# Optimization experiments

Measured on AMD Instinct MI355X. Metric: run time of the kernel, lower is better.

The kernel has to match this reference:

```python
import jax, jax.numpy as jnp
import numpy as np

N_NODES = 100000
N_EDGES = 1600000
F_IN = 128
HID = 64
EPS = 1e-5


def setup_inputs() -> dict:
    key = jax.random.key(0)
    ks = jax.random.split(key, 16)
    x = jax.random.normal(ks[0], (N_NODES, F_IN), dtype=jnp.float32)
    edge_index = jax.random.randint(ks[1], (2, N_EDGES), 0, N_NODES, dtype=jnp.int64)
    inp = {"x": x, "edge_index": edge_index}
    # GCN layers: layer 0 maps F_IN->HID, layers 1,2 map HID->HID
    dims = [(F_IN, HID), (HID, HID), (HID, HID)]
    for i, (fi, fo) in enumerate(dims):
        inp[f"W{i}"] = jax.random.normal(ks[2 + i], (fi, fo), dtype=jnp.float32) / np.sqrt(fi)
        inp[f"b{i}"] = jnp.zeros((fo,), dtype=jnp.float32)
        inp[f"g{i}"] = jnp.ones((fo,), dtype=jnp.float32)
        inp[f"bt{i}"] = jnp.zeros((fo,), dtype=jnp.float32)
    inp["lw1"] = jax.random.normal(ks[8], (HID, HID // 2), dtype=jnp.float32) / np.sqrt(HID)
    inp["lb1"] = jnp.zeros((HID // 2,), dtype=jnp.float32)
    inp["lw2"] = jax.random.normal(ks[9], (HID // 2, 1), dtype=jnp.float32) / np.sqrt(HID // 2)
    inp["lb2"] = jnp.zeros((1,), dtype=jnp.float32)
    return inp


def _gcn_norm(edge_index, n_nodes):
    # add self loops, symmetric normalization D^{-1/2}(A+I)D^{-1/2}
    loops = jnp.arange(n_nodes, dtype=edge_index.dtype)
    src = jnp.concatenate([edge_index[0], loops])
    dst = jnp.concatenate([edge_index[1], loops])
    deg = jax.ops.segment_sum(jnp.ones_like(dst, dtype=jnp.float32), dst, num_segments=n_nodes)
    dinv = jax.lax.rsqrt(deg)  # deg >= 1 thanks to self loops
    norm = dinv[src] * dinv[dst]  # [E+N]
    return src, dst, norm


def reference(x, edge_index, W0, b0, g0, bt0, W1, b1, g1, bt1, W2, b2, g2, bt2, lw1, lb1, lw2, lb2):
    n = x.shape[0]
    src, dst, norm = _gcn_norm(edge_index, n)
    layers = [(W0, b0, g0, bt0), (W1, b1, g1, bt1), (W2, b2, g2, bt2)]
    h = x
    for W, b, g, bt in layers:
        hw = h @ W                                  # [N, H] dense GEMM
        msg = hw[src] * norm[:, None]               # gather + scale, [E+N, H]
        agg = jax.ops.segment_sum(msg, dst, num_segments=n) + b  # scatter-add
        # BatchNorm1d (training-mode batch stats, biased var)
        mu = agg.mean(axis=0)
        var = agg.var(axis=0)
        h = (agg - mu) * jax.lax.rsqrt(var + EPS) * g + bt
        h = jax.nn.relu(h)                          # dropout = identity (inference)
    h = jax.nn.relu(h @ lw1 + lb1)
    out = h @ lw2 + lb2                             # [N, 1]
    return out[:, 0]
```

## Files before the change

### kernel.cpp

```cpp
#include <hip/hip_runtime.h>
#include <hip/hip_fp16.h>

#define HIDW 64
#define EPSV 1e-5f
#define CAP 32
#define GRP 512
#define CHUNK 4096
#define PSLOTS 40
#define NBIN_MAX 256
#define NCHUNK_MAX 512
#define NSLOT 64
#define OVFR 32768

__global__ __launch_bounds__(256) void k_zero(int* __restrict__ deg, int* __restrict__ ovfcnt,
                                              float* __restrict__ stats, int n) {
    int i = blockIdx.x * 256 + threadIdx.x;
    if (i < n) deg[i] = 0;
    if (i < 2) ovfcnt[i] = 0;
    if (i < 3 * NSLOT * 128) stats[i] = 0.f;
}

__global__ __launch_bounds__(256) void k_part(const int* __restrict__ srcv, const int* __restrict__ dstv,
                                              int2* __restrict__ pairs, unsigned char* __restrict__ cnts,
                                              int2* __restrict__ ovfl, int* __restrict__ ovfcnt,
                                              int e, int nchunk, int nbin) {
    __shared__ int lcnt[NBIN_MAX];
    int tid = threadIdx.x;
    int chunk = blockIdx.x;
    for (int i = tid; i < nbin; i += 256) lcnt[i] = 0;
    __syncthreads();
    int base = chunk * CHUNK;
#pragma unroll
    for (int t = 0; t < CHUNK / 256; ++t) {
        int i = base + t * 256 + tid;
        if (i < e) {
            int s = srcv[i];
            int d = dstv[i];
            int k = d >> 9;
            int slot = atomicAdd(&lcnt[k], 1);
            if (slot < PSLOTS) {
                pairs[((size_t)k * nchunk + chunk) * PSLOTS + slot] = make_int2(s, d);
            } else {
                int o = atomicAdd(&ovfcnt[0], 1);
                if (o < OVFR) ovfl[o] = make_int2(s, d);
            }
        }
    }
    __syncthreads();
    for (int i = tid; i < nbin; i += 256)
        cnts[(size_t)i * nchunk + chunk] = (unsigned char)min(lcnt[i], PSLOTS);
}

__global__ __launch_bounds__(256) void k_own(const int2* __restrict__ pairs, const unsigned char* __restrict__ cnts,
                                             int* __restrict__ deg, unsigned char* __restrict__ bcnt,
                                             int* __restrict__ csr, int2* __restrict__ ovfl,
                                             int* __restrict__ ovfcnt, int n, int nchunk) {
    __shared__ int lcnt[GRP];
    __shared__ int bkt[GRP * CAP];
    __shared__ unsigned char scnt[NCHUNK_MAX];
    int g = blockIdx.x;
    int tid = threadIdx.x;
    int nbase = g << 9;
    int nloc = min(GRP, n - nbase);
    for (int i = tid; i < GRP; i += 256) lcnt[i] = 0;
    for (int i = tid; i < nchunk; i += 256) scnt[i] = cnts[(size_t)g * nchunk + i];
    __syncthreads();
    const int2* pb = pairs + (size_t)g * nchunk * PSLOTS;
    int tot = nchunk * PSLOTS;
    for (int i = tid; i < tot; i += 256) {
        int c = i / PSLOTS;
        int s = i - c * PSLOTS;
        if (s < (int)scnt[c]) {
            int2 p = pb[i];
            int loc = p.y - nbase;
            int pos = atomicAdd(&lcnt[loc], 1);
            if (pos < CAP) {
                bkt[loc * CAP + pos] = p.x;
            } else {
                int o = atomicAdd(&ovfcnt[1], 1);
                if (o < OVFR) ovfl[OVFR + o] = p;
            }
        }
    }
    __syncthreads();
    int* csrb = csr + (size_t)nbase * CAP;
    for (int i = tid; i < nloc * CAP; i += 256) csrb[i] = bkt[i];
    for (int i = tid; i < nloc; i += 256) {
        int c = lcnt[i];
        deg[nbase + i] = c;
        bcnt[nbase + i] = (unsigned char)min(c, CAP);
    }
}

__global__ __launch_bounds__(256) void k_ovfdeg(const int2* __restrict__ ovfl, const int* __restrict__ ovfcnt,
                                                int* __restrict__ deg) {
    int m0 = min(ovfcnt[0], OVFR);
    for (int i = threadIdx.x; i < m0; i += 256) atomicAdd(&deg[ovfl[i].y], 1);
}

__global__ __launch_bounds__(256) void k_ovf(const __half* __restrict__ hw, const int2* __restrict__ ovfl,
                                             const int* __restrict__ ovfcnt, const int* __restrict__ deg,
                                             float* __restrict__ agg) {
    int m0 = min(ovfcnt[0], OVFR);
    int m1 = min(ovfcnt[1], OVFR);
    int tot = m0 + m1;
    if (tot == 0) return;
    int lane = threadIdx.x & 63;
    int w = (blockIdx.x * 256 + threadIdx.x) >> 6;
    for (; w < tot; w += gridDim.x * 4) {
        int2 p = (w < m0) ? ovfl[w] : ovfl[OVFR + (w - m0)];
        float wt = rsqrtf(1.0f + (float)deg[p.y]);
        atomicAdd(&agg[(size_t)p.y * HIDW + lane], __half2float(hw[(size_t)p.x * HIDW + lane]) * wt);
    }
}

__global__ __launch_bounds__(256) void k_count(const int* __restrict__ dstv, int* __restrict__ deg, int e) {
    int i = blockIdx.x * 256 + threadIdx.x;
    if (i < e) atomicAdd(&deg[dstv[i]], 1);
}

__global__ __launch_bounds__(256) void k_scan1(const int* __restrict__ deg, int* __restrict__ off,
                                               int* __restrict__ bsum, int n) {
    __shared__ int s[256];
    int tid = threadIdx.x;
    int i = blockIdx.x * 256 + tid;
    int v = (i < n) ? deg[i] : 0;
    s[tid] = v;
    __syncthreads();
    for (int o = 1; o < 256; o <<= 1) {
        int t = (tid >= o) ? s[tid - o] : 0;
        __syncthreads();
        s[tid] += t;
        __syncthreads();
    }
    if (i < n) off[i] = s[tid] - v;
    if (tid == 255) bsum[blockIdx.x] = s[255];
}

__global__ __launch_bounds__(512) void k_scan2(int* __restrict__ bsum, int nb) {
    __shared__ int s[512];
    int tid = threadIdx.x;
    int v = (tid < nb) ? bsum[tid] : 0;
    s[tid] = v;
    __syncthreads();
    for (int o = 1; o < 512; o <<= 1) {
        int t = (tid >= o) ? s[tid - o] : 0;
        __syncthreads();
        s[tid] += t;
        __syncthreads();
    }
    if (tid < nb) bsum[tid] = s[tid] - v;
}

__global__ __launch_bounds__(256) void k_scan3(int* __restrict__ off, const int* __restrict__ bsum, int n) {
    int i = blockIdx.x * 256 + threadIdx.x;
    if (i < n) off[i] += bsum[blockIdx.x];
}

__global__ __launch_bounds__(256) void k_fill2(const int* __restrict__ srcv, const int* __restrict__ dstv,
                                               int* __restrict__ roff, int* __restrict__ csr, int e) {
    int i = blockIdx.x * 256 + threadIdx.x;
    if (i < e) {
        int d = dstv[i];
        int p = atomicAdd(&roff[d], 1);
        csr[p] = srcv[i];
    }
}

template <int K, bool BN>
__global__ __launch_bounds__(256) void k_gemm(const float* __restrict__ h, const float* __restrict__ W,
                                              __half* __restrict__ hw, int n,
                                              const float* __restrict__ st, const float* __restrict__ g,
                                              const float* __restrict__ bt, float invn,
                                              const int* __restrict__ deg) {
    constexpr int KP = K + 4;
    constexpr int KQ = K / 4;
    __shared__ float sH[64 * KP];
    __shared__ float sW[K * 64];
    __shared__ float sM[128];
    __shared__ float sSc[HIDW];
    __shared__ float sSh[HIDW];
    int tid = threadIdx.x;
    int node0 = blockIdx.x * 64;

    if (BN) {
        if (tid < 128) {
            float t = 0.f;
#pragma unroll 8
            for (int s = 0; s < NSLOT; ++s) t += st[s * 128 + tid];
            sM[tid] = t;
        }
        __syncthreads();
        if (tid < HIDW) {
            float mu = sM[tid] * invn;
            float var = sM[HIDW + tid] * invn - mu * mu;
            var = fmaxf(var, 0.f);
            float rstd = rsqrtf(var + EPSV);
            float sc = rstd * g[tid];
            sSc[tid] = sc;
            sSh[tid] = bt[tid] - mu * sc;
        }
        __syncthreads();
    }

    for (int i = tid; i < K * 16; i += 256)
        ((float4*)sW)[i] = ((const float4*)W)[i];
    for (int i = tid; i < 64 * KQ; i += 256) {
        int row = i / KQ, kq = i % KQ;
        int nn = node0 + row;
        if (nn >= n) nn = n - 1;
        float4 v = ((const float4*)h)[(size_t)nn * KQ + kq];
        if (BN) {
            int c = 4 * kq;
            v.x = fmaxf(fmaf(v.x, sSc[c + 0], sSh[c + 0]), 0.f);
            v.y = fmaxf(fmaf(v.y, sSc[c + 1], sSh[c + 1]), 0.f);
            v.z = fmaxf(fmaf(v.z, sSc[c + 2], sSh[c + 2]), 0.f);
            v.w = fmaxf(fmaf(v.w, sSc[c + 3], sSh[c + 3]), 0.f);
        }
        ((float4*)(sH + row * KP))[kq] = v;
    }
    __syncthreads();

    int tx = tid & 15;
    int ny = tid >> 4;
    const float* hbase = sH + (4 * ny) * KP;

    float acc[4][4];
#pragma unroll
    for (int j = 0; j < 4; ++j)
#pragma unroll
        for (int c = 0; c < 4; ++c) acc[j][c] = 0.f;

#pragma unroll 2
    for (int kq = 0; kq < KQ; ++kq) {
        float4 w0 = ((const float4*)(sW + (4 * kq + 0) * 64))[tx];
        float4 w1 = ((const float4*)(sW + (4 * kq + 1) * 64))[tx];
        float4 w2 = ((const float4*)(sW + (4 * kq + 2) * 64))[tx];
        float4 w3 = ((const float4*)(sW + (4 * kq + 3) * 64))[tx];
#pragma unroll
        for (int j = 0; j < 4; ++j) {
            float4 hv = ((const float4*)(hbase + j * KP))[kq];
            acc[j][0] = fmaf(hv.x, w0.x, acc[j][0]);
            acc[j][1] = fmaf(hv.x, w0.y, acc[j][1]);
            acc[j][2] = fmaf(hv.x, w0.z, acc[j][2]);
            acc[j][3] = fmaf(hv.x, w0.w, acc[j][3]);
            acc[j][0] = fmaf(hv.y, w1.x, acc[j][0]);
            acc[j][1] = fmaf(hv.y, w1.y, acc[j][1]);
            acc[j][2] = fmaf(hv.y, w1.z, acc[j][2]);
            acc[j][3] = fmaf(hv.y, w1.w, acc[j][3]);
            acc[j][0] = fmaf(hv.z, w2.x, acc[j][0]);
            acc[j][1] = fmaf(hv.z, w2.y, acc[j][1]);
            acc[j][2] = fmaf(hv.z, w2.z, acc[j][2]);
            acc[j][3] = fmaf(hv.z, w2.w, acc[j][3]);
            acc[j][0] = fmaf(hv.w, w3.x, acc[j][0]);
            acc[j][1] = fmaf(hv.w, w3.y, acc[j][1]);
            acc[j][2] = fmaf(hv.w, w3.z, acc[j][2]);
            acc[j][3] = fmaf(hv.w, w3.w, acc[j][3]);
        }
    }

#pragma unroll
    for (int j = 0; j < 4; ++j) {
        int node = node0 + 4 * ny + j;
        if (node < n) {
            float dv = rsqrtf(1.0f + (float)deg[node]);
            __half2 p01 = __floats2half2_rn(acc[j][0] * dv, acc[j][1] * dv);
            __half2 p23 = __floats2half2_rn(acc[j][2] * dv, acc[j][3] * dv);
            uint2 r;
            r.x = *(unsigned int*)&p01;
            r.y = *(unsigned int*)&p23;
            ((uint2*)hw)[(size_t)node * 16 + tx] = r;
        }
    }
}

template <bool BUCKET>
__global__ __launch_bounds__(256) void k_gather(const __half* __restrict__ hw, const int* __restrict__ csr,
                                                const int* __restrict__ roff, const int* __restrict__ deg,
                                                const unsigned char* __restrict__ bcnt,
                                                const float* __restrict__ bias,
                                                float* __restrict__ agg, float* __restrict__ st, int n) {
    __shared__ float sS[4 * 64];
    __shared__ float sQ[4 * 64];
    int tid = threadIdx.x;
    int lane = tid & 63;
    int w = tid >> 6;
    int eh = lane >> 3;
    int c8 = lane & 7;
    int v = blockIdx.x * 4 + w;
    bool valid = (v < n);
    int vv = valid ? v : 0;
    int dcnt = deg[vv];
    float dv = rsqrtf(1.0f + (float)dcnt);
    int cnt;
    const int* base;
    if (BUCKET) {
        cnt = bcnt[vv];
        base = csr + (size_t)vv * CAP;
    } else {
        cnt = dcnt;
        base = csr + (roff[vv] - dcnt);
    }
    const char* hwb = (const char*)hw;

    float acc[8];
    {
        unsigned off0 = ((unsigned)vv << 7) + (c8 << 4);
        uint4 sv = *(const uint4*)(hwb + off0);
        const __half2* hp = (const __half2*)&sv;
#pragma unroll
        for (int i = 0; i < 4; ++i) {
            float2 f = __half22float2(hp[i]);
            acc[2 * i + 0] = (eh == 0) ? f.x : 0.f;
            acc[2 * i + 1] = (eh == 0) ? f.y : 0.f;
        }
    }

    for (int j0 = 0; j0 < cnt; j0 += 64) {
        int m = min(cnt - j0, 64);
        int idx = (lane < m) ? base[j0 + lane] : 0;
        int k = 0;
        for (; k + 16 <= m; k += 16) {
            int a0 = __shfl(idx, k + eh);
            int a1 = __shfl(idx, k + 8 + eh);
            uint4 v0 = *(const uint4*)(hwb + (((unsigned)a0 << 7) + (c8 << 4)));
            uint4 v1 = *(const uint4*)(hwb + (((unsigned)a1 << 7) + (c8 << 4)));
            const __half2* h0 = (const __half2*)&v0;
            const __half2* h1 = (const __half2*)&v1;
#pragma unroll
            for (int i = 0; i < 4; ++i) {
                float2 f0 = __half22float2(h0[i]);
                float2 f1 = __half22float2(h1[i]);
                acc[2 * i + 0] += f0.x + f1.x;
                acc[2 * i + 1] += f0.y + f1.y;
            }
        }
        for (; k < m; k += 8) {
            int a = __shfl(idx, k + eh);
            uint4 v0 = *(const uint4*)(hwb + (((unsigned)a << 7) + (c8 << 4)));
            if (k + eh < m) {
                const __half2* h0 = (const __half2*)&v0;
#pragma unroll
                for (int i = 0; i < 4; ++i) {
                    float2 f0 = __half22float2(h0[i]);
                    acc[2 * i + 0] += f0.x;
                    acc[2 * i + 1] += f0.y;
                }
            }
        }
    }
#pragma unroll
    for (int i = 0; i < 8; ++i) {
        acc[i] += __shfl_xor(acc[i], 8);
        acc[i] += __shfl_xor(acc[i], 16);
        acc[i] += __shfl_xor(acc[i], 32);
    }
    if (eh == 0) {
        float4 b0 = ((const float4*)bias)[c8 * 2 + 0];
        float4 b1 = ((const float4*)bias)[c8 * 2 + 1];
        float4 f0, f1;
        f0.x = fmaf(dv, acc[0], b0.x);
        f0.y = fmaf(dv, acc[1], b0.y);
        f0.z = fmaf(dv, acc[2], b0.z);
        f0.w = fmaf(dv, acc[3], b0.w);
        f1.x = fmaf(dv, acc[4], b1.x);
        f1.y = fmaf(dv, acc[5], b1.y);
        f1.z = fmaf(dv, acc[6], b1.z);
        f1.w = fmaf(dv, acc[7], b1.w);
        if (valid) {
            ((float4*)agg)[(size_t)vv * 16 + c8 * 2 + 0] = f0;
            ((float4*)agg)[(size_t)vv * 16 + c8 * 2 + 1] = f1;
        }
        float s0[8] = {f0.x, f0.y, f0.z, f0.w, f1.x, f1.y, f1.z, f1.w};
#pragma unroll
        for (int i = 0; i < 8; ++i) {
            float sv2 = valid ? s0[i] : 0.f;
            sS[w * 64 + c8 * 8 + i] = sv2;
            sQ[w * 64 + c8 * 8 + i] = sv2 * sv2;
        }
    }
    __syncthreads();
    if (tid < 64) {
        float S = sS[tid] + sS[64 + tid] + sS[128 + tid] + sS[192 + tid];
        float Q = sQ[tid] + sQ[64 + tid] + sQ[128 + tid] + sQ[192 + tid];
        float* slot = st + (size_t)(blockIdx.x & (NSLOT - 1)) * 128;
        atomicAdd(&slot[tid], S);
        atomicAdd(&slot[64 + tid], Q);
    }
}

__global__ __launch_bounds__(256) void k_head(const float* __restrict__ h, const float* __restrict__ lw1,
                                              const float* __restrict__ lb1, const float* __restrict__ lw2,
                                              const float* __restrict__ lb2, float* __restrict__ out, int n,
                                              const float* __restrict__ st, const float* __restrict__ g,
                                              const float* __restrict__ bt, float invn) {
    __shared__ float sW[64 * 32];
    __shared__ float sb1[32];
    __shared__ float sw2[32];
    __shared__ float sM[128];
    __shared__ float sSc[HIDW];
    __shared__ float sSh[HIDW];
    int tid = threadIdx.x;
    for (int i = tid; i < 64 * 32; i += 256) sW[i] = lw1[i];
    if (tid < 32) {
        sb1[tid] = lb1[tid];
        sw2[tid] = lw2[tid];
    }
    if (tid < 128) {
        float t = 0.f;
#pragma unroll 8
        for (int s = 0; s < NSLOT; ++s) t += st[s * 128 + tid];
        sM[tid] = t;
    }
    __syncthreads();
    if (tid < HIDW) {
        float mu = sM[tid] * invn;
        float var = sM[HIDW + tid] * invn - mu * mu;
        var = fmaxf(var, 0.f);
        float rstd = rsqrtf(var + EPSV);
        float sc = rstd * g[tid];
        sSc[tid] = sc;
        sSh[tid] = bt[tid] - mu * sc;
    }
    __syncthreads();
    int nd = blockIdx.x * 256 + tid;
    if (nd >= n) return;
    float acc[32];
#pragma unroll
    for (int j = 0; j < 32; ++j) acc[j] = sb1[j];
    const float4* hr = (const float4*)(h + (size_t)nd * HIDW);
#pragma unroll 4
    for (int kc = 0; kc < 16; ++kc) {
        float4 h4 = hr[kc];
        int c = 4 * kc;
        h4.x = fmaxf(fmaf(h4.x, sSc[c + 0], sSh[c + 0]), 0.f);
        h4.y = fmaxf(fmaf(h4.y, sSc[c + 1], sSh[c + 1]), 0.f);
        h4.z = fmaxf(fmaf(h4.z, sSc[c + 2], sSh[c + 2]), 0.f);
        h4.w = fmaxf(fmaf(h4.w, sSc[c + 3], sSh[c + 3]), 0.f);
        const float* w0 = &sW[(c + 0) * 32];
        const float* w1 = &sW[(c + 1) * 32];
        const float* w2 = &sW[(c + 2) * 32];
        const float* w3 = &sW[(c + 3) * 32];
#pragma unroll
        for (int j = 0; j < 32; ++j) {
            float t = fmaf(h4.x, w0[j], fmaf(h4.y, w1[j], fmaf(h4.z, w2[j], h4.w * w3[j])));
            acc[j] += t;
        }
    }
    float o = lb2[0];
#pragma unroll
    for (int j = 0; j < 32; ++j) o = fmaf(fmaxf(acc[j], 0.f), sw2[j], o);
    out[nd] = o;
}

extern "C" void kernel_launch(void* const* d_in, const int* in_sizes, int n_in,
                              void* d_out, int out_size, void* d_ws, size_t ws_size,
                              hipStream_t stream) {
    const float* x = (const float*)d_in[0];
    const int* ei = (const int*)d_in[1];
    const float* W[3] = {(const float*)d_in[2], (const float*)d_in[6], (const float*)d_in[10]};
    const float* B[3] = {(const float*)d_in[3], (const float*)d_in[7], (const float*)d_in[11]};
    const float* G[3] = {(const float*)d_in[4], (const float*)d_in[8], (const float*)d_in[12]};
    const float* BT[3] = {(const float*)d_in[5], (const float*)d_in[9], (const float*)d_in[13]};
    const float* lw1 = (const float*)d_in[14];
    const float* lb1 = (const float*)d_in[15];
    const float* lw2 = (const float*)d_in[16];
    const float* lb2 = (const float*)d_in[17];
    float* out = (float*)d_out;

    const int n = in_sizes[0] / 128;
    const int e = in_sizes[1] / 2;
    const int* srcv = ei;
    const int* dstv = ei + e;
    const float invn = 1.0f / (float)n;
    const int nchunk = (e + CHUNK - 1) / CHUNK;
    const int nbin = (n + GRP - 1) / GRP;

    char* ws = (char*)d_ws;
    size_t off = 0;
    auto alloc = [&](size_t bytes) -> char* {
        off = (off + 511) & ~(size_t)511;
        char* p = ws + off;
        off += bytes;
        return p;
    };
    float* stats = (float*)alloc((size_t)3 * NSLOT * 128 * 4);
    int* ovfcnt = (int*)alloc(512);
    int2* ovfl = (int2*)alloc((size_t)2 * OVFR * 8);
    unsigned char* cnts = (unsigned char*)alloc((size_t)nbin * nchunk);
    unsigned char* bcnt = (unsigned char*)alloc((size_t)n);
    int* deg = (int*)alloc((size_t)n * 4);
    float* bufA = (float*)alloc((size_t)n * HIDW * 4);
    __half* bufB = (__half*)alloc((size_t)n * HIDW * 2);
    size_t commonOff = off;

    size_t needA = ((commonOff + 511) & ~(size_t)511) + (size_t)n * CAP * 4;
    size_t pairsBytes = (size_t)nbin * nchunk * PSLOTS * 8;
    bool useA = (needA <= ws_size) && (pairsBytes <= (size_t)n * HIDW * 4) &&
                (nchunk <= NCHUNK_MAX) && (nbin <= NBIN_MAX);

    const int gN = (n + 255) / 256;
    const int gG = (n + 63) / 64;
    const int gV = (n + 3) / 4;

    int2* pairs = (int2*)bufA;
    int* csrB = nullptr;
    int* roff = nullptr;
    int* bsum = nullptr;
    int* csrC = nullptr;

    if (useA) {
        csrB = (int*)alloc((size_t)n * CAP * 4);
        k_zero<<<gN, 256, 0, stream>>>(deg, ovfcnt, stats, n);
        k_part<<<nchunk, 256, 0, stream>>>(srcv, dstv, pairs, cnts, ovfl, ovfcnt, e, nchunk, nbin);
        k_own<<<nbin, 256, 0, stream>>>(pairs, cnts, deg, bcnt, csrB, ovfl, ovfcnt, n, nchunk);
        k_ovfdeg<<<1, 256, 0, stream>>>(ovfl, ovfcnt, deg);
    } else {
        roff = (int*)alloc((size_t)(n + 1) * 4);
        bsum = (int*)alloc(512 * 4);
        csrC = (int*)alloc((size_t)e * 4);
        k_zero<<<gN, 256, 0, stream>>>(deg, ovfcnt, stats, n);
        k_count<<<(e + 255) / 256, 256, 0, stream>>>(dstv, deg, e);
        k_scan1<<<gN, 256, 0, stream>>>(deg, roff, bsum, n);
        k_scan2<<<1, 512, 0, stream>>>(bsum, gN);
        k_scan3<<<gN, 256, 0, stream>>>(roff, bsum, n);
        k_fill2<<<(e + 255) / 256, 256, 0, stream>>>(srcv, dstv, roff, csrC, e);
    }

    for (int L = 0; L < 3; ++L) {
        float* stL = stats + (size_t)L * NSLOT * 128;
        if (L == 0)
            k_gemm<128, false><<<gG, 256, 0, stream>>>(x, W[0], bufB, n, nullptr, nullptr, nullptr, invn, deg);
        else
            k_gemm<64, true><<<gG, 256, 0, stream>>>(bufA, W[L], bufB, n, stats + (size_t)(L - 1) * NSLOT * 128,
                                                     G[L - 1], BT[L - 1], invn, deg);
        if (useA) {
            k_gather<true><<<gV, 256, 0, stream>>>(bufB, csrB, nullptr, deg, bcnt, B[L], bufA, stL, n);
            k_ovf<<<16, 256, 0, stream>>>(bufB, ovfl, ovfcnt, deg, bufA);
        } else {
            k_gather<false><<<gV, 256, 0, stream>>>(bufB, csrC, roff, deg, nullptr, B[L], bufA, stL, n);
        }
    }

    k_head<<<gN, 256, 0, stream>>>(bufA, lw1, lb1, lw2, lb2, out, n, stats + (size_t)2 * NSLOT * 128,
                                   G[2], BT[2], invn);
}
```

Before: 397.2 us.

## Map eight nodes per wavefront in bucketed gather kernel

Replaces the one-node-per-wavefront gather on the bucketed CSR path with a kernel where each 8-lane group owns one node and walks its neighbor list serially, two edges per iteration. The old version split each node's edges across 8 lane groups and then reduced across them. The new mapping is meant to remove that cross-lane reduction and the idle lanes for low-degree nodes (average degree about 16), and to reduce the block count by a factor of 8. In exchange, lanes in a wavefront diverge when degrees differ, since the loop runs to the maximum count among the 8 nodes. The non-bucketed fallback path is only renamed.

```diff
diff --git a/kernel.cpp b/kernel.cpp
--- a/kernel.cpp
+++ b/kernel.cpp
@@ -274,12 +274,134 @@
     }
 }
 
-template <bool BUCKET>
-__global__ __launch_bounds__(256) void k_gather(const __half* __restrict__ hw, const int* __restrict__ csr,
-                                                const int* __restrict__ roff, const int* __restrict__ deg,
-                                                const unsigned char* __restrict__ bcnt,
-                                                const float* __restrict__ bias,
-                                                float* __restrict__ agg, float* __restrict__ st, int n) {
+__global__ __launch_bounds__(256) void k_gath8(const __half* __restrict__ hw, const int* __restrict__ csr,
+                                               const int* __restrict__ deg, const unsigned char* __restrict__ bcnt,
+                                               const float* __restrict__ bias,
+                                               float* __restrict__ agg, float* __restrict__ st, int n) {
+    __shared__ float sS[4 * 64];
+    __shared__ float sQ[4 * 64];
+    int tid = threadIdx.x;
+    int lane = tid & 63;
+    int w = tid >> 6;
+    int g = lane >> 3;
+    int p = lane & 7;
+    int v = (blockIdx.x * 4 + w) * 8 + g;
+    bool valid = (v < n);
+    int vv = valid ? v : 0;
+    int dcnt = deg[vv];
+    int cnt = valid ? (int)bcnt[vv] : 0;
+    float dv = rsqrtf(1.0f + (float)dcnt);
+    const int* base = csr + (size_t)vv * CAP;
+    const char* hwb = (const char*)hw;
+
+    float4 b0 = ((const float4*)bias)[p * 2 + 0];
+    float4 b1 = ((const float4*)bias)[p * 2 + 1];
+
+    float acc[8];
+    {
+        uint4 sv = make_uint4(0, 0, 0, 0);
+        if (valid) sv = *(const uint4*)(hwb + (((unsigned)vv << 7) + (p << 4)));
+        const __half2* hp = (const __half2*)&sv;
+#pragma unroll
+        for (int i = 0; i < 4; ++i) {
+            float2 f = __half22float2(hp[i]);
+            acc[2 * i + 0] = f.x;
+            acc[2 * i + 1] = f.y;
+        }
+    }
+
+    int mc = cnt;
+    mc = max(mc, __shfl_xor(mc, 8));
+    mc = max(mc, __shfl_xor(mc, 16));
+    mc = max(mc, __shfl_xor(mc, 32));
+
+    int j = 0;
+    for (; j + 2 <= mc; j += 2) {
+        bool a0 = (j < cnt), a1 = (j + 1 < cnt);
+        int i0 = 0, i1 = 0;
+        if (a0) i0 = base[j];
+        if (a1) i1 = base[j + 1];
+        uint4 r0 = make_uint4(0, 0, 0, 0), r1 = make_uint4(0, 0, 0, 0);
+        if (a0) r0 = *(const uint4*)(hwb + (((unsigned)i0 << 7) + (p << 4)));
+        if (a1) r1 = *(const uint4*)(hwb + (((unsigned)i1 << 7) + (p << 4)));
+        const __half2* h0 = (const __half2*)&r0;
+        const __half2* h1 = (const __half2*)&r1;
+#pragma unroll
+        for (int i = 0; i < 4; ++i) {
+            float2 f0 = __half22float2(h0[i]);
+            float2 f1 = __half22float2(h1[i]);
+            acc[2 * i + 0] += f0.x + f1.x;
+            acc[2 * i + 1] += f0.y + f1.y;
+        }
+    }
+    if (j < mc) {
+        bool a0 = (j < cnt);
+        int i0 = 0;
+        if (a0) i0 = base[j];
+        uint4 r0 = make_uint4(0, 0, 0, 0);
+        if (a0) r0 = *(const uint4*)(hwb + (((unsigned)i0 << 7) + (p << 4)));
+        const __half2* h0 = (const __half2*)&r0;
+#pragma unroll
+        for (int i = 0; i < 4; ++i) {
+            float2 f0 = __half22float2(h0[i]);
+            acc[2 * i + 0] += f0.x;
+            acc[2 * i + 1] += f0.y;
+        }
+    }
+
+    float fin[8];
+    fin[0] = fmaf(dv, acc[0], b0.x);
+    fin[1] = fmaf(dv, acc[1], b0.y);
+    fin[2] = fmaf(dv, acc[2], b0.z);
+    fin[3] = fmaf(dv, acc[3], b0.w);
+    fin[4] = fmaf(dv, acc[4], b1.x);
+    fin[5] = fmaf(dv, acc[5], b1.y);
+    fin[6] = fmaf(dv, acc[6], b1.z);
+    fin[7] = fmaf(dv, acc[7], b1.w);
+    if (valid) {
+        float4 o0 = make_float4(fin[0], fin[1], fin[2], fin[3]);
+        float4 o1 = make_float4(fin[4], fin[5], fin[6], fin[7]);
+        float4* ap = (float4*)(agg + (size_t)vv * HIDW + p * 8);
+        ap[0] = o0;
+        ap[1] = o1;
+    }
+    float sv2[8], qv2[8];
+#pragma unroll
+    for (int i = 0; i < 8; ++i) {
+        float t = valid ? fin[i] : 0.f;
+        sv2[i] = t;
+        qv2[i] = t * t;
+    }
+#pragma unroll
+    for (int i = 0; i < 8; ++i) {
+        sv2[i] += __shfl_xor(sv2[i], 8);
+        qv2[i] += __shfl_xor(qv2[i], 8);
+        sv2[i] += __shfl_xor(sv2[i], 16);
+        qv2[i] += __shfl_xor(qv2[i], 16);
+        sv2[i] += __shfl_xor(sv2[i], 32);
+        qv2[i] += __shfl_xor(qv2[i], 32);
+    }
+    if (g == 0) {
+#pragma unroll
+        for (int i = 0; i < 8; ++i) {
+            sS[w * 64 + p * 8 + i] = sv2[i];
+            sQ[w * 64 + p * 8 + i] = qv2[i];
+        }
+    }
+    __syncthreads();
+    if (tid < 64) {
+        float S = sS[tid] + sS[64 + tid] + sS[128 + tid] + sS[192 + tid];
+        float Q = sQ[tid] + sQ[64 + tid] + sQ[128 + tid] + sQ[192 + tid];
+        float* slot = st + (size_t)(blockIdx.x & (NSLOT - 1)) * 128;
+        atomicAdd(&slot[tid], S);
+        atomicAdd(&slot[64 + tid], Q);
+    }
+}
+
+__global__ __launch_bounds__(256) void k_gatherB(const __half* __restrict__ hw, const int* __restrict__ csr,
+                                                 const int* __restrict__ roff, const int* __restrict__ deg,
+                                                 const float* __restrict__ bias,
+                                                 float* __restrict__ agg, float* __restrict__ st, int n) {
     __shared__ float sS[4 * 64];
     __shared__ float sQ[4 * 64];
     int tid = threadIdx.x;
@@ -292,15 +414,8 @@
     int vv = valid ? v : 0;
     int dcnt = deg[vv];
     float dv = rsqrtf(1.0f + (float)dcnt);
-    int cnt;
-    const int* base;
-    if (BUCKET) {
-        cnt = bcnt[vv];
-        base = csr + (size_t)vv * CAP;
-    } else {
-        cnt = dcnt;
-        base = csr + (roff[vv] - dcnt);
-    }
+    int cnt = dcnt;
+    const int* base = csr + (roff[vv] - dcnt);
     const char* hwb = (const char*)hw;
 
     float acc[8];
@@ -502,6 +617,7 @@
     const int gN = (n + 255) / 256;
     const int gG = (n + 63) / 64;
     const int gV = (n + 3) / 4;
+    const int gV8 = (n + 31) / 32;
 
     int2* pairs = (int2*)bufA;
     int* csrB = nullptr;
@@ -535,10 +651,10 @@
             k_gemm<64, true><<<gG, 256, 0, stream>>>(bufA, W[L], bufB, n, stats + (size_t)(L - 1) * NSLOT * 128,
                                                      G[L - 1], BT[L - 1], invn, deg);
         if (useA) {
-            k_gather<true><<<gV, 256, 0, stream>>>(bufB, csrB, nullptr, deg, bcnt, B[L], bufA, stL, n);
+            k_gath8<<<gV8, 256, 0, stream>>>(bufB, csrB, deg, bcnt, B[L], bufA, stL, n);
             k_ovf<<<16, 256, 0, stream>>>(bufB, ovfl, ovfcnt, deg, bufA);
         } else {
-            k_gather<false><<<gV, 256, 0, stream>>>(bufB, csrC, roff, deg, nullptr, B[L], bufA, stL, n);
+            k_gatherB<<<gV, 256, 0, stream>>>(bufB, csrC, roff, deg, B[L], bufA, stL, n);
         }
     }
 
```

Result: no change. 392.3 us (-1.2%).
